# Kernel optimization log

Measured on AMD Instinct MI355X. Metric: run time of the kernel, lower is better.

The kernel has to match this reference:

```python
import jax, jax.numpy as jnp
import numpy as np

B, IN, OUT, E, CTX, DEMO = 32768, 512, 128, 16, 256, 16
HID = IN // 2
GATE_IN = CTX + IN + DEMO  # 784


def setup_inputs() -> dict:
    key = jax.random.key(0)
    ks = jax.random.split(key, 9)
    inp = {
        'x': jax.random.normal(ks[0], (B, IN), dtype=jnp.float32),
        'u': jax.random.normal(ks[1], (B, CTX), dtype=jnp.float32),
        'd': jax.random.normal(ks[2], (B, DEMO), dtype=jnp.float32),
        # gate Linear(GATE_IN -> E)
        'gate_W': jax.random.normal(ks[3], (E, GATE_IN), dtype=jnp.float32) * 0.02,
        'gate_b': jnp.zeros((E,), dtype=jnp.float32),
        # per-expert MLP: Linear(IN->HID), ReLU, Linear(HID->OUT); stacked over experts
        'W1': jax.random.normal(ks[4], (E, HID, IN), dtype=jnp.float32) * 0.02,
        'b1': jnp.zeros((E, HID), dtype=jnp.float32),
        'W2': jax.random.normal(ks[5], (E, OUT, HID), dtype=jnp.float32) * 0.02,
        'b2': jnp.zeros((E, OUT), dtype=jnp.float32),
    }
    return inp


def reference(x, u, d, gate_W, gate_b, W1, b1, W2, b2):
    # gate input = cat([u, x, d], dim=1)  -> [B, GATE_IN]
    g_in = jnp.concatenate([u, x, d], axis=1)
    gate_logits = g_in @ gate_W.T + gate_b            # [B, E]
    weights = jax.nn.softmax(gate_logits, axis=1)     # [B, E]
    # all-expert MLP as batched GEMMs
    h = jax.nn.relu(jnp.einsum('bi,ehi->beh', x, W1) + b1[None])   # [B, E, HID]
    expert_outputs = jnp.einsum('beh,eoh->beo', h, W2) + b2[None]  # [B, E, OUT]
    # mixture_mode == 'logits': weighted sum over experts
    out = jnp.einsum('be,beo->bo', weights, expert_outputs)        # [B, OUT]
    return out
```

## Files before the change

kernel.cpp:

```cpp
#include <hip/hip_runtime.h>

#define B_    32768
#define IN_   512
#define HID_  256
#define OUT_  128
#define E_    16
#define CTX_  256
#define DEMO_ 16
#define GIN_  784

typedef __attribute__((ext_vector_type(8))) short short8;
typedef __attribute__((ext_vector_type(4))) float floatx4;

__device__ __forceinline__ short f2bf(float x){
  unsigned u = __builtin_bit_cast(unsigned, x);
  u += 0x7FFFu + ((u >> 16) & 1u);
  return (short)(u >> 16);
}

__device__ __forceinline__ short8 pack8(float4 a, float4 b){
  short8 r;
  r[0]=f2bf(a.x); r[1]=f2bf(a.y); r[2]=f2bf(a.z); r[3]=f2bf(a.w);
  r[4]=f2bf(b.x); r[5]=f2bf(b.y); r[6]=f2bf(b.z); r[7]=f2bf(b.w);
  return r;
}

__device__ __forceinline__ void load_lds16(const short* g, short* l){
  __builtin_amdgcn_global_load_lds((const __attribute__((address_space(1))) void*)g,
                                   (__attribute__((address_space(3))) void*)l,
                                   16, 0, 0);
}

__device__ __forceinline__ void stage128x64(short* lds, const short* g, int gpitch, int tid){
  const int wvv = tid >> 6, ln = tid & 63;
  const int cb = ln & 7, rsub = ln >> 3;
  #pragma unroll
  for (int i = 0; i < 4; ++i){
    const int r0  = (wvv*4 + i)*8;
    const int row = r0 + rsub;
    const short* gp = g + (size_t)row*gpitch + ((cb ^ rsub) << 3);
    load_lds16(gp, lds + r0*64);
  }
}

__global__ void convert_kernel(const float* __restrict__ x, const float* __restrict__ w1,
                               const float* __restrict__ w2, short* __restrict__ xb,
                               short* __restrict__ w1b, short* __restrict__ w2b){
  const int N1 = B_*IN_, N2 = E_*HID_*IN_, N3 = E_*OUT_*HID_;
  const int total4 = (N1 + N2 + N3) >> 2;
  for (int i = blockIdx.x*blockDim.x + threadIdx.x; i < total4; i += gridDim.x*blockDim.x){
    int e4 = i << 2;
    const float* src; short* dst; int off;
    if (e4 < N1)            { src = x;  dst = xb;  off = e4; }
    else if (e4 < N1 + N2)  { src = w1; dst = w1b; off = e4 - N1; }
    else                    { src = w2; dst = w2b; off = e4 - (N1 + N2); }
    float4 v = *(const float4*)(src + off);
    *(short4*)(dst + off) = make_short4(f2bf(v.x), f2bf(v.y), f2bf(v.z), f2bf(v.w));
  }
}

__global__ __launch_bounds__(256)
void gate_kernel(const float* __restrict__ u, const short* __restrict__ xb,
                 const float* __restrict__ d, const float* __restrict__ gW,
                 const float* __restrict__ gb, float* __restrict__ wout){
  const int tid  = threadIdx.x;
  const int wave = tid >> 6, lane = tid & 63;
  const int l15  = lane & 15, quad = lane >> 4;
  const int row0 = blockIdx.x*64 + wave*16;
  const int rA   = row0 + l15;
  const int kq   = quad*8;

  floatx4 acc  = {0.f,0.f,0.f,0.f};
  floatx4 acc2 = {0.f,0.f,0.f,0.f};

  #pragma unroll
  for (int t = 0; t < 8; ++t){
    const float4 a0 = *(const float4*)&u[(size_t)rA*CTX_ + t*32 + kq];
    const float4 a1 = *(const float4*)&u[(size_t)rA*CTX_ + t*32 + kq + 4];
    const float4 b0 = *(const float4*)&gW[(size_t)l15*GIN_ + t*32 + kq];
    const float4 b1 = *(const float4*)&gW[(size_t)l15*GIN_ + t*32 + kq + 4];
    acc = __builtin_amdgcn_mfma_f32_16x16x32_bf16(pack8(a0,a1), pack8(b0,b1), acc, 0,0,0);
  }
  #pragma unroll
  for (int t = 0; t < 16; ++t){
    const short8 af = *(const short8*)&xb[(size_t)rA*IN_ + t*32 + kq];
    const float4 b0 = *(const float4*)&gW[(size_t)l15*GIN_ + 256 + t*32 + kq];
    const float4 b1 = *(const float4*)&gW[(size_t)l15*GIN_ + 256 + t*32 + kq + 4];
    acc2 = __builtin_amdgcn_mfma_f32_16x16x32_bf16(af, pack8(b0,b1), acc2, 0,0,0);
  }
  {
    short8 af = {0,0,0,0,0,0,0,0}, bf = {0,0,0,0,0,0,0,0};
    if (quad < 2){
      const float4 a0 = *(const float4*)&d[(size_t)rA*DEMO_ + kq];
      const float4 a1 = *(const float4*)&d[(size_t)rA*DEMO_ + kq + 4];
      const float4 b0 = *(const float4*)&gW[(size_t)l15*GIN_ + 768 + kq];
      const float4 b1 = *(const float4*)&gW[(size_t)l15*GIN_ + 768 + kq + 4];
      af = pack8(a0,a1); bf = pack8(b0,b1);
    }
    acc = __builtin_amdgcn_mfma_f32_16x16x32_bf16(af, bf, acc, 0,0,0);
  }

  const float bias = gb[l15];
  #pragma unroll
  for (int r = 0; r < 4; ++r){
    float v = acc[r] + acc2[r] + bias;
    float m = v;
    #pragma unroll
    for (int s = 1; s <= 8; s <<= 1) m = fmaxf(m, __shfl_xor(m, s));
    const float p = __expf(v - m);
    float ssum = p;
    #pragma unroll
    for (int s = 1; s <= 8; s <<= 1) ssum += __shfl_xor(ssum, s);
    wout[(size_t)(row0 + quad*4 + r)*E_ + l15] = p / ssum;
  }
}

__global__ __launch_bounds__(256, 2)
void moe_kernel(const short* __restrict__ xb, const short* __restrict__ w1b,
                const short* __restrict__ w2b, const float* __restrict__ gatew,
                const float* __restrict__ b1g, const float* __restrict__ b2g,
                float* __restrict__ out){
  __shared__ alignas(16) char smem[51200];
  short* s_x  = (short*)smem;
  short* s_w1 = (short*)(smem + 16384);
  short* s_h  = (short*)smem;
  short* s_w2 = (short*)(smem + 34816);

  const int tid  = threadIdx.x;
  const int wv   = tid >> 6;
  const int lane = tid & 63;
  const int l15  = lane & 15;
  const int hi2  = lane >> 4;
  const int h_off  = (wv >> 1) * 64;
  const int mb_off = (wv & 1) * 64;
  const int m_off  = (wv >> 1) * 64;
  const int o_off  = (wv & 1) * 64;
  const int blk_m0 = blockIdx.x * 128;
  const int eg = blockIdx.y;

  floatx4 oacc[4][4];
  #pragma unroll
  for (int a = 0; a < 4; ++a)
    #pragma unroll
    for (int b = 0; b < 4; ++b) oacc[a][b] = floatx4{0.f,0.f,0.f,0.f};

  if (eg == 0){
    #pragma unroll 1
    for (int e = 0; e < E_; ++e){
      float b2v[4];
      #pragma unroll
      for (int nt = 0; nt < 4; ++nt) b2v[nt] = b2g[e*OUT_ + o_off + nt*16 + l15];
      #pragma unroll
      for (int mt = 0; mt < 4; ++mt){
        #pragma unroll
        for (int r = 0; r < 4; ++r){
          const float wgt = gatew[(size_t)(blk_m0 + m_off + mt*16 + hi2*4 + r)*E_ + e];
          #pragma unroll
          for (int nt = 0; nt < 4; ++nt) oacc[mt][nt][r] += wgt * b2v[nt];
        }
      }
    }
  }

  #pragma unroll 1
  for (int ei = 0; ei < 4; ++ei){
    const int e = eg*4 + ei;
    #pragma unroll 1
    for (int half = 0; half < 2; ++half){
      floatx4 g1[4][4];
      #pragma unroll
      for (int a = 0; a < 4; ++a)
        #pragma unroll
        for (int b = 0; b < 4; ++b) g1[a][b] = floatx4{0.f,0.f,0.f,0.f};

      const short* w1base = w1b + (size_t)(e*HID_ + half*128) * IN_;
      #pragma unroll 1
      for (int kc = 0; kc < 8; ++kc){
        stage128x64(s_x,  xb + (size_t)blk_m0*IN_ + kc*64, IN_, tid);
        stage128x64(s_w1, w1base + kc*64, IN_, tid);
        __syncthreads();
        #pragma unroll
        for (int ks = 0; ks < 2; ++ks){
          const int kb = ks*4 + hi2;
          const int sw = (kb ^ (l15 & 7)) << 3;
          short8 af[4], bf[4];
          #pragma unroll
          for (int ht = 0; ht < 4; ++ht)
            af[ht] = *(const short8*)&s_w1[(h_off + ht*16 + l15)*64 + sw];
          #pragma unroll
          for (int mt = 0; mt < 4; ++mt)
            bf[mt] = *(const short8*)&s_x[(mb_off + mt*16 + l15)*64 + sw];
          #pragma unroll
          for (int ht = 0; ht < 4; ++ht)
            #pragma unroll
            for (int mt = 0; mt < 4; ++mt)
              g1[ht][mt] = __builtin_amdgcn_mfma_f32_16x16x32_bf16(af[ht], bf[mt], g1[ht][mt], 0,0,0);
        }
        __syncthreads();
      }

      const short* w2base = w2b + (size_t)e*OUT_*HID_ + half*128;
      stage128x64(s_w2, w2base, HID_, tid);

      {
        float4 b1v[4];
        #pragma unroll
        for (int ht = 0; ht < 4; ++ht)
          b1v[ht] = *(const float4*)&b1g[e*HID_ + half*128 + h_off + ht*16 + hi2*4];
        float wgt[4];
        #pragma unroll
        for (int mt = 0; mt < 4; ++mt)
          wgt[mt] = gatew[(size_t)(blk_m0 + mb_off + mt*16 + l15)*E_ + e];
        #pragma unroll
        for (int ht = 0; ht < 4; ++ht){
          const float b1r[4] = {b1v[ht].x, b1v[ht].y, b1v[ht].z, b1v[ht].w};
          #pragma unroll
          for (int mt = 0; mt < 4; ++mt){
            short4 pk;
            float v0 = fmaxf(g1[ht][mt][0] + b1r[0], 0.f) * wgt[mt];
            float v1 = fmaxf(g1[ht][mt][1] + b1r[1], 0.f) * wgt[mt];
            float v2 = fmaxf(g1[ht][mt][2] + b1r[2], 0.f) * wgt[mt];
            float v3 = fmaxf(g1[ht][mt][3] + b1r[3], 0.f) * wgt[mt];
            pk.x = f2bf(v0); pk.y = f2bf(v1); pk.z = f2bf(v2); pk.w = f2bf(v3);
            *(short4*)&s_h[(size_t)(mb_off + mt*16 + l15)*136 + h_off + ht*16 + hi2*4] = pk;
          }
        }
      }
      __syncthreads();

      #pragma unroll 1
      for (int kc2 = 0; kc2 < 2; ++kc2){
        #pragma unroll
        for (int ks = 0; ks < 2; ++ks){
          const int kb = ks*4 + hi2;
          const int kk = kc2*64 + (kb << 3);
          const int sw = (kb ^ (l15 & 7)) << 3;
          short8 af[4], bf[4];
          #pragma unroll
          for (int mt = 0; mt < 4; ++mt)
            af[mt] = *(const short8*)&s_h[(m_off + mt*16 + l15)*136 + kk];
          #pragma unroll
          for (int nt = 0; nt < 4; ++nt)
            bf[nt] = *(const short8*)&s_w2[(o_off + nt*16 + l15)*64 + sw];
          #pragma unroll
          for (int mt = 0; mt < 4; ++mt)
            #pragma unroll
            for (int nt = 0; nt < 4; ++nt)
              oacc[mt][nt] = __builtin_amdgcn_mfma_f32_16x16x32_bf16(af[mt], bf[nt], oacc[mt][nt], 0,0,0);
        }
        __syncthreads();
        if (kc2 == 0){
          stage128x64(s_w2, w2base + 64, HID_, tid);
          __syncthreads();
        }
      }
    }
  }

  #pragma unroll
  for (int mt = 0; mt < 4; ++mt)
    #pragma unroll
    for (int nt = 0; nt < 4; ++nt)
      #pragma unroll
      for (int r = 0; r < 4; ++r)
        atomicAdd(&out[(size_t)(blk_m0 + m_off + mt*16 + hi2*4 + r)*OUT_ + o_off + nt*16 + l15],
                  oacc[mt][nt][r]);
}

extern "C" void kernel_launch(void* const* d_in, const int* in_sizes, int n_in,
                              void* d_out, int out_size, void* d_ws, size_t ws_size,
                              hipStream_t stream){
  const float* x  = (const float*)d_in[0];
  const float* u  = (const float*)d_in[1];
  const float* dd = (const float*)d_in[2];
  const float* gW = (const float*)d_in[3];
  const float* gb = (const float*)d_in[4];
  const float* W1 = (const float*)d_in[5];
  const float* b1 = (const float*)d_in[6];
  const float* W2 = (const float*)d_in[7];
  const float* b2 = (const float*)d_in[8];
  float* out = (float*)d_out;

  short* xb  = (short*)d_ws;
  short* w1b = xb  + (size_t)B_*IN_;
  short* w2b = w1b + (size_t)E_*HID_*IN_;
  float* gw  = (float*)(w2b + (size_t)E_*OUT_*HID_);

  hipMemsetAsync(d_out, 0, (size_t)B_*OUT_*sizeof(float), stream);
  hipLaunchKernelGGL(convert_kernel, dim3(4096), dim3(256), 0, stream, x, W1, W2, xb, w1b, w2b);
  hipLaunchKernelGGL(gate_kernel, dim3(B_/64), dim3(256), 0, stream, u, xb, dd, gW, gb, gw);
  hipLaunchKernelGGL(moe_kernel, dim3(B_/128, 4), dim3(256), 0, stream, xb, w1b, w2b, gw, b1, b2, out);
  (void)in_sizes; (void)n_in; (void)out_size; (void)ws_size;
}
```

Measured before the change: 383.4 us.

## Load W2 fragments directly into registers and swizzle hidden tile in LDS

W2 operands for the second GEMM are now read straight from global memory into registers (16 short8 per lane), so they are no longer staged through shared memory. This drops two LDS staging passes and their barriers per expert-half. The hidden activation tile moves from a padded stride-136 layout to a stride-128 XOR-swizzled layout, and shared memory shrinks from 51200 to 32768 bytes. The extra 64 VGPRs for W2 fragments could raise register pressure under launch_bounds(256,2), and the uncoalesced global loads depend on L2 hits.

```diff
diff --git a/kernel.cpp b/kernel.cpp
--- a/kernel.cpp
+++ b/kernel.cpp
@@ -120,11 +120,10 @@
                 const short* __restrict__ w2b, const float* __restrict__ gatew,
                 const float* __restrict__ b1g, const float* __restrict__ b2g,
                 float* __restrict__ out){
-  __shared__ alignas(16) char smem[51200];
+  __shared__ alignas(16) char smem[32768];
   short* s_x  = (short*)smem;
   short* s_w1 = (short*)(smem + 16384);
   short* s_h  = (short*)smem;
-  short* s_w2 = (short*)(smem + 34816);
 
   const int tid  = threadIdx.x;
   const int wv   = tid >> 6;
@@ -199,8 +198,15 @@
         __syncthreads();
       }
 
-      const short* w2base = w2b + (size_t)e*OUT_*HID_ + half*128;
-      stage128x64(s_w2, w2base, HID_, tid);
+      short8 w2f[4][4];
+      {
+        const short* w2p = w2b + (size_t)e*OUT_*HID_ + half*128;
+        #pragma unroll
+        for (int ks = 0; ks < 4; ++ks)
+          #pragma unroll
+          for (int nt = 0; nt < 4; ++nt)
+            w2f[ks][nt] = *(const short8*)&w2p[(size_t)(o_off + nt*16 + l15)*HID_ + ks*32 + hi2*8];
+      }
 
       {
         float4 b1v[4];
@@ -214,46 +220,38 @@
         #pragma unroll
         for (int ht = 0; ht < 4; ++ht){
           const float b1r[4] = {b1v[ht].x, b1v[ht].y, b1v[ht].z, b1v[ht].w};
+          const int hb = ((h_off + ht*16) >> 3) + (hi2 >> 1);
+          const int sub = (hi2 & 1) * 4;
           #pragma unroll
           for (int mt = 0; mt < 4; ++mt){
+            const int m = mb_off + mt*16 + l15;
             short4 pk;
-            float v0 = fmaxf(g1[ht][mt][0] + b1r[0], 0.f) * wgt[mt];
-            float v1 = fmaxf(g1[ht][mt][1] + b1r[1], 0.f) * wgt[mt];
-            float v2 = fmaxf(g1[ht][mt][2] + b1r[2], 0.f) * wgt[mt];
-            float v3 = fmaxf(g1[ht][mt][3] + b1r[3], 0.f) * wgt[mt];
-            pk.x = f2bf(v0); pk.y = f2bf(v1); pk.z = f2bf(v2); pk.w = f2bf(v3);
-            *(short4*)&s_h[(size_t)(mb_off + mt*16 + l15)*136 + h_off + ht*16 + hi2*4] = pk;
+            pk.x = f2bf(fmaxf(g1[ht][mt][0] + b1r[0], 0.f) * wgt[mt]);
+            pk.y = f2bf(fmaxf(g1[ht][mt][1] + b1r[1], 0.f) * wgt[mt]);
+            pk.z = f2bf(fmaxf(g1[ht][mt][2] + b1r[2], 0.f) * wgt[mt]);
+            pk.w = f2bf(fmaxf(g1[ht][mt][3] + b1r[3], 0.f) * wgt[mt]);
+            *(short4*)&s_h[m*128 + ((hb ^ (m & 7)) << 3) + sub] = pk;
           }
         }
       }
       __syncthreads();
 
-      #pragma unroll 1
-      for (int kc2 = 0; kc2 < 2; ++kc2){
-        #pragma unroll
-        for (int ks = 0; ks < 2; ++ks){
-          const int kb = ks*4 + hi2;
-          const int kk = kc2*64 + (kb << 3);
-          const int sw = (kb ^ (l15 & 7)) << 3;
-          short8 af[4], bf[4];
-          #pragma unroll
-          for (int mt = 0; mt < 4; ++mt)
-            af[mt] = *(const short8*)&s_h[(m_off + mt*16 + l15)*136 + kk];
+      #pragma unroll
+      for (int ks = 0; ks < 4; ++ks){
+        short8 af[4];
+        #pragma unroll
+        for (int mt = 0; mt < 4; ++mt){
+          const int m = m_off + mt*16 + l15;
+          const int hbL = ks*4 + hi2;
+          af[mt] = *(const short8*)&s_h[m*128 + ((hbL ^ (m & 7)) << 3)];
+        }
+        #pragma unroll
+        for (int mt = 0; mt < 4; ++mt)
           #pragma unroll
           for (int nt = 0; nt < 4; ++nt)
-            bf[nt] = *(const short8*)&s_w2[(o_off + nt*16 + l15)*64 + sw];
-          #pragma unroll
-          for (int mt = 0; mt < 4; ++mt)
-            #pragma unroll
-            for (int nt = 0; nt < 4; ++nt)
-              oacc[mt][nt] = __builtin_amdgcn_mfma_f32_16x16x32_bf16(af[mt], bf[nt], oacc[mt][nt], 0,0,0);
-        }
-        __syncthreads();
-        if (kc2 == 0){
-          stage128x64(s_w2, w2base + 64, HID_, tid);
-          __syncthreads();
-        }
-      }
+            oacc[mt][nt] = __builtin_amdgcn_mfma_f32_16x16x32_bf16(af[mt], w2f[ks][nt], oacc[mt][nt], 0,0,0);
+      }
+      __syncthreads();
     }
   }
 
```

New measurement: 465.8 us. +21.5%, slower.
